# Kernel optimization log

Hardware: AMD Instinct MI355X
Metric: run time of the kernel (lower is better)

## Reference

```python
import jax, jax.numpy as jnp
import numpy as np

B, T_ENC, D_IN, H, C, STEPS = 512, 64, 512, 512, 38, 26


def setup_inputs() -> dict:
    key = jax.random.key(0)
    ks = jax.random.split(key, 12)
    s = 0.05
    return {
        "encoder_output": jax.random.normal(ks[0], (B, T_ENC, D_IN), jnp.float32),
        "text": jax.random.randint(ks[1], (B, STEPS), 0, C),
        "w_i2h": jax.random.normal(ks[2], (H, D_IN), jnp.float32) * s,
        "w_h2h": jax.random.normal(ks[3], (H, H), jnp.float32) * s,
        "b_h2h": jax.random.normal(ks[4], (H,), jnp.float32) * s,
        "w_score": jax.random.normal(ks[5], (1, H), jnp.float32) * s,
        "w_ih": jax.random.normal(ks[6], (4 * H, D_IN + C), jnp.float32) * s,
        "w_hh": jax.random.normal(ks[7], (4 * H, H), jnp.float32) * s,
        "b_ih": jax.random.normal(ks[8], (4 * H,), jnp.float32) * s,
        "b_hh": jax.random.normal(ks[9], (4 * H,), jnp.float32) * s,
        "w_gen": jax.random.normal(ks[10], (C, H), jnp.float32) * s,
        "b_gen": jax.random.normal(ks[11], (C,), jnp.float32) * s,
    }


def reference(encoder_output, text, w_i2h, w_h2h, b_h2h, w_score, w_ih, w_hh,
              b_ih, b_hh, w_gen, b_gen):
    # i2h(batch_H) is step-invariant -> hoist out of the decode loop (same math).
    H_proj = jnp.einsum('btd,hd->bth', encoder_output, w_i2h)  # [B,T,H]
    onehots = jax.nn.one_hot(text, C, dtype=encoder_output.dtype)  # [B,S,C]
    oh_seq = jnp.swapaxes(onehots, 0, 1)  # [S,B,C]

    def step(carry, oh):
        h, c = carry
        hp = (h @ w_h2h.T + b_h2h)[:, None, :]                 # [B,1,H]
        e = jnp.tanh(H_proj + hp) @ w_score[0]                  # [B,T]
        alpha = jax.nn.softmax(e, axis=1)                       # [B,T]
        context = jnp.einsum('bt,btd->bd', alpha, encoder_output)
        x = jnp.concatenate([context, oh], axis=1)              # [B,D+C]
        gates = x @ w_ih.T + b_ih + h @ w_hh.T + b_hh           # [B,4H]
        i_g, f_g, g_g, o_g = jnp.split(gates, 4, axis=1)
        c_new = jax.nn.sigmoid(f_g) * c + jax.nn.sigmoid(i_g) * jnp.tanh(g_g)
        h_new = jax.nn.sigmoid(o_g) * jnp.tanh(c_new)
        return (h_new, c_new), h_new

    z = jnp.zeros((encoder_output.shape[0], w_h2h.shape[0]), encoder_output.dtype)
    _, hs = jax.lax.scan(step, (z, z), oh_seq)                  # hs: [S,B,H]
    hiddens = jnp.swapaxes(hs, 0, 1)                            # [B,S,H]
    probs = hiddens @ w_gen.T + b_gen                           # [B,S,C]
    return probs
```

## Files before the change

### kernel.cpp

```cpp
#include <hip/hip_runtime.h>

typedef __attribute__((ext_vector_type(8))) short bf16x8;
typedef __attribute__((ext_vector_type(4))) float f32x4;
typedef __attribute__((ext_vector_type(4))) int   i32x4;

#define DEV static __device__ __forceinline__

constexpr int BATCH = 512;
constexpr int TENC  = 64;
constexpr int DIN   = 512;
constexpr int HDIM  = 512;
constexpr int NCLS  = 38;
constexpr int STEPS = 26;
constexpr int NG    = 4 * HDIM;

constexpr size_t HP_OFF   = 0;
constexpr size_t HP_SZ    = (size_t)BATCH * TENC * HDIM * 2;
constexpr size_t ENC_OFF  = HP_OFF + HP_SZ;
constexpr size_t ENC_SZ   = (size_t)BATCH * TENC * DIN * 2;
constexpr size_t A2_OFF   = ENC_OFF + ENC_SZ;
constexpr size_t A2_SZ    = (size_t)2 * BATCH * 1024 * 2;
constexpr size_t HP32_OFF = A2_OFF + A2_SZ;
constexpr size_t HP32_SZ  = (size_t)BATCH * HDIM * 4;
constexpr size_t B2R_OFF  = HP32_OFF + HP32_SZ;
constexpr size_t B2R_SZ   = (size_t)NG * 1024 * 2;
constexpr size_t WI2H_OFF = B2R_OFF + B2R_SZ;
constexpr size_t WI2H_SZ  = (size_t)HDIM * DIN * 2;
constexpr size_t B3_OFF   = WI2H_OFF + WI2H_SZ;
constexpr size_t B3_SZ    = (size_t)576 * HDIM * 2;
constexpr size_t WOH_OFF  = B3_OFF + B3_SZ;
constexpr size_t WOH_SZ   = (size_t)NG * NCLS * 4;
constexpr size_t BIAS_OFF = WOH_OFF + WOH_SZ;
constexpr size_t BIAS_SZ  = (size_t)NG * 4;
constexpr size_t HSEQ_OFF = BIAS_OFF + BIAS_SZ;
constexpr size_t HSEQ_SZ  = (size_t)STEPS * BATCH * HDIM * 2;
constexpr size_t BAR_OFF  = HSEQ_OFF + HSEQ_SZ;
constexpr size_t BAR_SZ   = 16384;

DEV float bf2f(unsigned short s) {
    unsigned u = ((unsigned)s) << 16;
    return __builtin_bit_cast(float, u);
}
DEV unsigned short f2bf(float f) {
    unsigned u = __builtin_bit_cast(unsigned, f);
    u = (u + 0x7fffu + ((u >> 16) & 1u)) >> 16;
    return (unsigned short)u;
}
DEV float sigmoid_f(float x) { return 1.f / (1.f + __expf(-x)); }
DEV float tanh_f(float x) {
    x = fminf(fmaxf(x, -15.f), 15.f);
    float e = __expf(2.f * x);
    return (e - 1.f) / (e + 1.f);
}

DEV unsigned aload(const unsigned* p) {
    return __hip_atomic_load(p, __ATOMIC_RELAXED, __HIP_MEMORY_SCOPE_AGENT);
}
DEV unsigned long long aload64(const unsigned long long* p) {
    return __hip_atomic_load(p, __ATOMIC_RELAXED, __HIP_MEMORY_SCOPE_AGENT);
}
DEV float aloadf(const float* p) {
    return __hip_atomic_load(p, __ATOMIC_RELAXED, __HIP_MEMORY_SCOPE_AGENT);
}
DEV void astore(unsigned* p, unsigned v) {
    __hip_atomic_store(p, v, __ATOMIC_RELAXED, __HIP_MEMORY_SCOPE_AGENT);
}
DEV void astoref(float* p, float v) {
    __hip_atomic_store(p, v, __ATOMIC_RELAXED, __HIP_MEMORY_SCOPE_AGENT);
}
DEV bf16x8 mk_frag(unsigned long long lo, unsigned long long hi) {
    union { unsigned long long q[2]; bf16x8 v; } u;
    u.q[0] = lo; u.q[1] = hi;
    return u.v;
}

DEV void gbar(unsigned* bar, int bid) {
    __syncthreads();
    if (threadIdx.x == 0) {
        const int sg = bid & 31;
        unsigned* sub  = bar + sg * 32;
        unsigned* root = bar + 1024;
        unsigned* genp = bar + 1056 + sg * 32;
        unsigned g = aload(genp);
        bool flipped = false;
        if (__hip_atomic_fetch_add(sub, 1u, __ATOMIC_RELAXED, __HIP_MEMORY_SCOPE_AGENT) == 7u) {
            if (__hip_atomic_fetch_add(root, 1u, __ATOMIC_RELAXED, __HIP_MEMORY_SCOPE_AGENT) == 31u) {
                #pragma unroll
                for (int i = 0; i < 32; i++) astore(bar + i * 32, 0u);
                astore(root, 0u);
                asm volatile("s_waitcnt vmcnt(0)" ::: "memory");
                #pragma unroll
                for (int i = 0; i < 32; i++) astore(bar + 1056 + i * 32, g + 1u);
                flipped = true;
            }
        }
        if (!flipped) {
            while (aload(genp) == g) __builtin_amdgcn_s_sleep(1);
        }
    }
    __syncthreads();
}

__global__ void conv_bf16_kernel(const float* __restrict__ in,
                                 unsigned short* __restrict__ out, int n4) {
    int i = blockIdx.x * blockDim.x + threadIdx.x;
    int stride = gridDim.x * blockDim.x;
    for (; i < n4; i += stride) {
        float4 v = ((const float4*)in)[i];
        ushort4 o;
        o.x = f2bf(v.x); o.y = f2bf(v.y); o.z = f2bf(v.z); o.w = f2bf(v.w);
        ((ushort4*)out)[i] = o;
    }
}

__global__ void build_b2r_kernel(const float* __restrict__ w_ih, const float* __restrict__ w_hh,
                                 const float* __restrict__ b_ih, const float* __restrict__ b_hh,
                                 unsigned short* __restrict__ B2r, float* __restrict__ woh,
                                 float* __restrict__ bias2r) {
    int np = blockIdx.x;
    int u = np >> 2, g = np & 3;
    int src = g * 512 + u;
    for (int k = threadIdx.x; k < 512; k += blockDim.x) {
        B2r[np * 1024 + k]       = f2bf(w_ih[src * 550 + k]);
        B2r[np * 1024 + 512 + k] = f2bf(w_hh[src * 512 + k]);
    }
    if (threadIdx.x < NCLS) woh[np * NCLS + threadIdx.x] = w_ih[src * 550 + 512 + threadIdx.x];
    if (threadIdx.x == 0)   bias2r[np] = b_ih[src] + b_hh[src];
}

__global__ void build_b3_kernel(const float* __restrict__ w_h2h, const float* __restrict__ w_gen,
                                unsigned short* __restrict__ B3) {
    int n = blockIdx.x;
    for (int k = threadIdx.x; k < 512; k += blockDim.x) {
        float v = 0.f;
        if (n < 512)      v = w_h2h[n * 512 + k];
        else if (n < 550) v = w_gen[(n - 512) * 512 + k];
        B3[n * 512 + k] = f2bf(v);
    }
}

__global__ void init_state_kernel(float* __restrict__ hp32,
                                  unsigned short* __restrict__ A2,
                                  const float* __restrict__ b_h2h,
                                  unsigned* __restrict__ bar) {
    int b = blockIdx.x;
    for (int j = threadIdx.x; j < 512; j += blockDim.x) {
        hp32[b * 512 + j] = b_h2h[j];
        A2[b * 1024 + 512 + j] = 0;
    }
    if (b == 0)
        for (int j = threadIdx.x; j < 2112; j += blockDim.x) bar[j] = 0;
}

template<int BM, int BN, int WN, int FRM, int FRN>
DEV void gemm_core(const unsigned short* __restrict__ A, int ldA,
                   const unsigned short* __restrict__ Bm, int ldB, int K,
                   int m0, int n0, unsigned short* __restrict__ lA,
                   unsigned short* __restrict__ lB, f32x4 acc[FRM][FRN]) {
    constexpr int LSTR = 40;
    const int tid  = threadIdx.x;
    const int lane = tid & 63;
    const int wid  = tid >> 6;
    const int wm = wid / WN, wn = wid % WN;
    const int fr_row = lane & 15;
    const int fr_kb  = (lane >> 4) * 8;

    for (int k0 = 0; k0 < K; k0 += 32) {
        for (int u = tid; u < BM * 4; u += 256) {
            int r = u >> 2, cb = u & 3;
            *(i32x4*)(lA + r * LSTR + cb * 8) =
                *(const i32x4*)(A + (size_t)(m0 + r) * ldA + k0 + cb * 8);
        }
        for (int u = tid; u < BN * 4; u += 256) {
            int r = u >> 2, cb = u & 3;
            *(i32x4*)(lB + r * LSTR + cb * 8) =
                *(const i32x4*)(Bm + (size_t)(n0 + r) * ldB + k0 + cb * 8);
        }
        __syncthreads();
        bf16x8 af[FRM], bfv[FRN];
        #pragma unroll
        for (int i = 0; i < FRM; i++)
            af[i] = *(const bf16x8*)(lA + (wm * FRM * 16 + i * 16 + fr_row) * LSTR + fr_kb);
        #pragma unroll
        for (int j = 0; j < FRN; j++)
            bfv[j] = *(const bf16x8*)(lB + (wn * FRN * 16 + j * 16 + fr_row) * LSTR + fr_kb);
        #pragma unroll
        for (int i = 0; i < FRM; i++)
            #pragma unroll
            for (int j = 0; j < FRN; j++)
                acc[i][j] = __builtin_amdgcn_mfma_f32_16x16x32_bf16(af[i], bfv[j], acc[i][j], 0, 0, 0);
        __syncthreads();
    }
}

__global__ __launch_bounds__(256) void gemm_bf16out_kernel(
    const unsigned short* __restrict__ A, int ldA,
    const unsigned short* __restrict__ Bm, int ldB,
    unsigned short* __restrict__ C, int ldC, int K) {
    constexpr int BM = 128, BN = 128, FRM = 4, FRN = 4;
    __shared__ __align__(16) unsigned short lA[BM * 40], lB[BN * 40];
    int m0 = blockIdx.x * BM, n0 = blockIdx.y * BN;
    f32x4 acc[FRM][FRN] = {};
    gemm_core<BM, BN, 2, FRM, FRN>(A, ldA, Bm, ldB, K, m0, n0, lA, lB, acc);
    const int lane = threadIdx.x & 63, wid = threadIdx.x >> 6;
    const int wm = wid >> 1, wn = wid & 1;
    #pragma unroll
    for (int i = 0; i < FRM; i++)
        #pragma unroll
        for (int j = 0; j < FRN; j++)
            #pragma unroll
            for (int r = 0; r < 4; r++) {
                int m = m0 + wm * FRM * 16 + i * 16 + (lane >> 4) * 4 + r;
                int n = n0 + wn * FRN * 16 + j * 16 + (lane & 15);
                C[(size_t)m * ldC + n] = f2bf(acc[i][j][r]);
            }
}

__global__ __launch_bounds__(256) void probs_kernel(
    const unsigned short* __restrict__ hseq,
    const unsigned short* __restrict__ Bg,
    const float* __restrict__ b_gen, float* __restrict__ out) {
    __shared__ __align__(16) unsigned short lA[64 * 40], lB[64 * 40];
    int m0 = blockIdx.x * 64;
    f32x4 acc[2][2] = {};
    gemm_core<64, 64, 2, 2, 2>(hseq, 512, Bg, 512, 512, m0, 0, lA, lB, acc);
    const int lane = threadIdx.x & 63, wid = threadIdx.x >> 6;
    const int wm = wid >> 1, wn = wid & 1;
    #pragma unroll
    for (int i = 0; i < 2; i++)
        #pragma unroll
        for (int j = 0; j < 2; j++)
            #pragma unroll
            for (int r = 0; r < 4; r++) {
                int m = m0 + wm * 32 + i * 16 + (lane >> 4) * 4 + r;
                int n = wn * 32 + j * 16 + (lane & 15);
                if (n < NCLS) {
                    int ss = m >> 9, b = m & 511;
                    out[((size_t)b * STEPS + ss) * NCLS + n] = acc[i][j][r] + b_gen[n];
                }
            }
}

__global__ __launch_bounds__(512, 2) void decode_kernel(
    const unsigned short* __restrict__ Hp,
    const unsigned short* __restrict__ enc,
    unsigned short* __restrict__ A2,
    float* __restrict__ hp32,
    const unsigned short* __restrict__ B2r,
    const float* __restrict__ bias2r,
    const float* __restrict__ woh,
    const unsigned short* __restrict__ B3,
    const float* __restrict__ b_h2h,
    const float* __restrict__ w_score,
    const int* __restrict__ text,
    unsigned short* __restrict__ hseq,
    unsigned* __restrict__ bar) {
    __shared__ __align__(16) unsigned short lB2[32 * 1032];
    __shared__ __align__(16) unsigned short lB3[32 * 520];
    __shared__ __align__(16) char scr[18432];

    const int bid  = blockIdx.x;
    const int tid  = threadIdx.x;
    const int lane = tid & 63, wid = tid >> 6;

    const int nb = bid & 63;
    const int mb = bid >> 6;
    const int n3 = bid & 15;
    const int m3 = bid >> 4;

    for (int u = tid; u < 4096; u += 512) {
        int r = u >> 7, cb = u & 127;
        *(i32x4*)(lB2 + r * 1032 + cb * 8) =
            *(const i32x4*)(B2r + (size_t)(nb * 32 + r) * 1024 + cb * 8);
    }
    for (int u = tid; u < 2048; u += 512) {
        int r = u >> 6, cb = u & 63;
        *(i32x4*)(lB3 + r * 520 + cb * 8) =
            *(const i32x4*)(B3 + (size_t)(n3 * 32 + r) * 512 + cb * 8);
    }

    float c0 = 0.f, c1 = 0.f;

    for (int s = 0; s < STEPS; ++s) {
        unsigned short* A2cur = A2 + (size_t)(s & 1) * BATCH * 1024;
        unsigned short* A2nxt = A2 + (size_t)((s + 1) & 1) * BATCH * 1024;

        {
            float* e_lds  = (float*)scr;
            float* al_lds = e_lds + 128;
            const int half = tid >> 8, t4 = tid & 255, w4 = t4 >> 6;
            const int b = bid * 2 + half;
            float hp8[8], ws8[8];
            const float* hpr = hp32 + b * 512 + lane * 8;
            #pragma unroll
            for (int j = 0; j < 8; j++) hp8[j] = aloadf(hpr + j);
            {
                const float4* wsp = (const float4*)(w_score + lane * 8);
                float4 w0 = wsp[0], w1 = wsp[1];
                ws8[0] = w0.x; ws8[1] = w0.y; ws8[2] = w0.z; ws8[3] = w0.w;
                ws8[4] = w1.x; ws8[5] = w1.y; ws8[6] = w1.z; ws8[7] = w1.w;
            }
            for (int t = w4; t < 64; t += 4) {
                bf16x8 hv = *(const bf16x8*)(Hp + ((size_t)b * 64 + t) * 512 + lane * 8);
                float a = 0.f;
                #pragma unroll
                for (int j = 0; j < 8; j++)
                    a += ws8[j] * tanh_f(hp8[j] + bf2f((unsigned short)hv[j]));
                #pragma unroll
                for (int off = 32; off > 0; off >>= 1) a += __shfl_down(a, off);
                if (lane == 0) e_lds[half * 64 + t] = a;
            }
            __syncthreads();
            if (w4 == 0) {
                float v = e_lds[half * 64 + lane];
                float m = v;
                #pragma unroll
                for (int off = 32; off > 0; off >>= 1) m = fmaxf(m, __shfl_xor(m, off));
                float ex = __expf(v - m);
                float sum = ex;
                #pragma unroll
                for (int off = 32; off > 0; off >>= 1) sum += __shfl_xor(sum, off);
                al_lds[half * 64 + lane] = ex / sum;
            }
            __syncthreads();
            float a0 = 0.f, a1 = 0.f;
            const unsigned short* erow = enc + (size_t)b * 64 * 512 + t4 * 2;
            #pragma unroll 8
            for (int t = 0; t < 64; t++) {
                float al = al_lds[half * 64 + t];
                unsigned pv = *(const unsigned*)(erow + (size_t)t * 512);
                a0 += al * bf2f((unsigned short)(pv & 0xffffu));
                a1 += al * bf2f((unsigned short)(pv >> 16));
            }
            unsigned pk = ((unsigned)f2bf(a1) << 16) | (unsigned)f2bf(a0);
            astore((unsigned*)(A2cur + (size_t)b * 1024) + t4, pk);
        }
        gbar(bar, bid);

        {
            const int m0 = mb * 128;
            const unsigned long long* Ab = (const unsigned long long*)
                (A2cur + (size_t)(m0 + wid * 16 + (lane & 15)) * 1024 + (lane >> 4) * 8);
            const unsigned short* lb0 = lB2 + (lane & 15) * 1032 + (lane >> 4) * 8;
            const unsigned short* lb1 = lb0 + 16 * 1032;
            f32x4 acc0 = {}, acc1 = {};
            #pragma unroll
            for (int hf = 0; hf < 2; ++hf) {
                unsigned long long a0v[16], a1v[16];
                #pragma unroll
                for (int kc = 0; kc < 16; ++kc) {
                    a0v[kc] = aload64(Ab + (hf * 16 + kc) * 8);
                    a1v[kc] = aload64(Ab + (hf * 16 + kc) * 8 + 1);
                }
                #pragma unroll
                for (int kc = 0; kc < 16; ++kc) {
                    bf16x8 af = mk_frag(a0v[kc], a1v[kc]);
                    bf16x8 b0 = *(const bf16x8*)(lb0 + (hf * 16 + kc) * 32);
                    bf16x8 b1 = *(const bf16x8*)(lb1 + (hf * 16 + kc) * 32);
                    acc0 = __builtin_amdgcn_mfma_f32_16x16x32_bf16(af, b0, acc0, 0, 0, 0);
                    acc1 = __builtin_amdgcn_mfma_f32_16x16x32_bf16(af, b1, acc1, 0, 0, 0);
                }
            }
            float* gbuf = (float*)scr;
            const int grow = wid * 16 + (lane >> 4) * 4;
            const int gcol = lane & 15;
            #pragma unroll
            for (int r = 0; r < 4; r++) {
                gbuf[(grow + r) * 36 + gcol]      = acc0[r];
                gbuf[(grow + r) * 36 + 16 + gcol] = acc1[r];
            }
            __syncthreads();
            {
                const int rl = tid >> 2, q = tid & 3;
                const int b = m0 + rl;
                const int npb = nb * 32 + q * 8;
                const int u0 = npb >> 2;
                const int tb = text[b * STEPS + s];
                const float* gr = gbuf + rl * 36 + q * 8;
                float4 g0 = *(const float4*)gr;
                float4 g1 = *(const float4*)(gr + 4);
                float vi0 = g0.x + bias2r[npb + 0] + woh[(npb + 0) * NCLS + tb];
                float vf0 = g0.y + bias2r[npb + 1] + woh[(npb + 1) * NCLS + tb];
                float vg0 = g0.z + bias2r[npb + 2] + woh[(npb + 2) * NCLS + tb];
                float vo0 = g0.w + bias2r[npb + 3] + woh[(npb + 3) * NCLS + tb];
                float vi1 = g1.x + bias2r[npb + 4] + woh[(npb + 4) * NCLS + tb];
                float vf1 = g1.y + bias2r[npb + 5] + woh[(npb + 5) * NCLS + tb];
                float vg1 = g1.z + bias2r[npb + 6] + woh[(npb + 6) * NCLS + tb];
                float vo1 = g1.w + bias2r[npb + 7] + woh[(npb + 7) * NCLS + tb];
                float cn0 = sigmoid_f(vf0) * c0 + sigmoid_f(vi0) * tanh_f(vg0);
                float cn1 = sigmoid_f(vf1) * c1 + sigmoid_f(vi1) * tanh_f(vg1);
                c0 = cn0; c1 = cn1;
                float hn0 = sigmoid_f(vo0) * tanh_f(cn0);
                float hn1 = sigmoid_f(vo1) * tanh_f(cn1);
                unsigned hp2 = ((unsigned)f2bf(hn1) << 16) | (unsigned)f2bf(hn0);
                astore((unsigned*)(A2nxt + (size_t)b * 1024 + 512 + u0), hp2);
                *(unsigned*)(hseq + ((size_t)s * BATCH + b) * 512 + u0) = hp2;
            }
        }

        if (s + 1 < STEPS) {
            gbar(bar, bid);
            {
                const int wi = wid & 3, kl = wid >> 2;
                const int tm = (wi >> 1) * 16, tn = (wi & 1) * 16;
                const int m0 = m3 * 32, nc = n3 * 32;
                const unsigned long long* Ab = (const unsigned long long*)
                    (A2nxt + (size_t)(m0 + tm + (lane & 15)) * 1024 + 512 + kl * 256 + (lane >> 4) * 8);
                const unsigned short* lbr = lB3 + (tn + (lane & 15)) * 520 + kl * 256 + (lane >> 4) * 8;
                unsigned long long a0v[8], a1v[8];
                #pragma unroll
                for (int kc = 0; kc < 8; ++kc) {
                    a0v[kc] = aload64(Ab + kc * 8);
                    a1v[kc] = aload64(Ab + kc * 8 + 1);
                }
                f32x4 acc = {};
                #pragma unroll
                for (int kc = 0; kc < 8; ++kc) {
                    bf16x8 af = mk_frag(a0v[kc], a1v[kc]);
                    bf16x8 bf = *(const bf16x8*)(lbr + kc * 32);
                    acc = __builtin_amdgcn_mfma_f32_16x16x32_bf16(af, bf, acc, 0, 0, 0);
                }
                float* pbuf = (float*)scr;
                if (kl == 1) {
                    #pragma unroll
                    for (int r = 0; r < 4; r++)
                        pbuf[wi * 272 + ((lane >> 4) * 4 + r) * 17 + (lane & 15)] = acc[r];
                }
                __syncthreads();
                if (kl == 0) {
                    #pragma unroll
                    for (int r = 0; r < 4; r++) {
                        int row = (lane >> 4) * 4 + r, col = lane & 15;
                        float v = acc[r] + pbuf[wi * 272 + row * 17 + col] + b_h2h[nc + tn + col];
                        astoref(hp32 + (size_t)(m0 + tm + row) * 512 + nc + tn + col, v);
                    }
                }
            }
            gbar(bar, bid);
        }
    }
}

extern "C" void kernel_launch(void* const* d_in, const int* in_sizes, int n_in,
                              void* d_out, int out_size, void* d_ws, size_t ws_size,
                              hipStream_t stream) {
    (void)in_sizes; (void)n_in; (void)out_size; (void)ws_size;
    const float* enc_f   = (const float*)d_in[0];
    const int*   text    = (const int*)d_in[1];
    const float* w_i2h   = (const float*)d_in[2];
    const float* w_h2h   = (const float*)d_in[3];
    const float* b_h2h   = (const float*)d_in[4];
    const float* w_score = (const float*)d_in[5];
    const float* w_ih    = (const float*)d_in[6];
    const float* w_hh    = (const float*)d_in[7];
    const float* b_ih    = (const float*)d_in[8];
    const float* b_hh    = (const float*)d_in[9];
    const float* w_gen   = (const float*)d_in[10];
    const float* b_gen   = (const float*)d_in[11];
    float* out = (float*)d_out;

    char* ws = (char*)d_ws;
    const unsigned short* Hp     = (const unsigned short*)(ws + HP_OFF);
    unsigned short*       Hp_w   = (unsigned short*)(ws + HP_OFF);
    const unsigned short* encb   = (const unsigned short*)(ws + ENC_OFF);
    unsigned short*       encb_w = (unsigned short*)(ws + ENC_OFF);
    unsigned short*       A2     = (unsigned short*)(ws + A2_OFF);
    float*                hp32   = (float*)(ws + HP32_OFF);
    const unsigned short* B2r    = (const unsigned short*)(ws + B2R_OFF);
    unsigned short*       B2r_w  = (unsigned short*)(ws + B2R_OFF);
    unsigned short*       wi2hb  = (unsigned short*)(ws + WI2H_OFF);
    const unsigned short* B3     = (const unsigned short*)(ws + B3_OFF);
    unsigned short*       B3_w   = (unsigned short*)(ws + B3_OFF);
    const float*          woh    = (const float*)(ws + WOH_OFF);
    float*                woh_w  = (float*)(ws + WOH_OFF);
    const float*          bias2r = (const float*)(ws + BIAS_OFF);
    float*                bias2r_w = (float*)(ws + BIAS_OFF);
    unsigned short*       hseq   = (unsigned short*)(ws + HSEQ_OFF);
    unsigned*             bar    = (unsigned*)(ws + BAR_OFF);

    conv_bf16_kernel<<<2048, 256, 0, stream>>>(enc_f, encb_w, BATCH * TENC * DIN / 4);
    conv_bf16_kernel<<<256, 256, 0, stream>>>(w_i2h, wi2hb, HDIM * DIN / 4);
    build_b2r_kernel<<<NG, 256, 0, stream>>>(w_ih, w_hh, b_ih, b_hh, B2r_w, woh_w, bias2r_w);
    build_b3_kernel<<<576, 256, 0, stream>>>(w_h2h, w_gen, B3_w);
    init_state_kernel<<<BATCH, 256, 0, stream>>>(hp32, A2, b_h2h, bar);

    gemm_bf16out_kernel<<<dim3(BATCH * TENC / 128, HDIM / 128), 256, 0, stream>>>(
        encb, DIN, wi2hb, DIN, Hp_w, HDIM, DIN);

    {
        void* args[13] = {
            (void*)&Hp, (void*)&encb, (void*)&A2, (void*)&hp32,
            (void*)&B2r, (void*)&bias2r, (void*)&woh, (void*)&B3,
            (void*)&b_h2h, (void*)&w_score, (void*)&text, (void*)&hseq, (void*)&bar
        };
        hipLaunchCooperativeKernel((const void*)decode_kernel, dim3(256), dim3(512),
                                   args, 0, stream);
    }

    probs_kernel<<<dim3(STEPS * BATCH / 64), 256, 0, stream>>>(
        hseq, B3 + (size_t)512 * 512, b_gen, out);
}
```

Before: 1.358 ms.

## Precompute recurrent gate GEMM half before barrier and use monotonic grid barrier

Moves the h_prev × W_hh half of the gate MFMA accumulation ahead of the attention phase so it overlaps with attention work instead of following the grid barrier. The grid barrier is rewritten to use monotonically increasing generation counters, dropping the per-barrier reset stores and sleep in the spin loop. This relies on the barrier memory being zeroed at each launch and adds register pressure from holding accumulators across the attention phase.

```diff
diff --git a/kernel.cpp b/kernel.cpp
--- a/kernel.cpp
+++ b/kernel.cpp
@@ -74,29 +74,20 @@
     return u.v;
 }
 
-DEV void gbar(unsigned* bar, int bid) {
+DEV void gbar(unsigned* bar, int bid, unsigned g) {
     __syncthreads();
     if (threadIdx.x == 0) {
         const int sg = bid & 31;
         unsigned* sub  = bar + sg * 32;
         unsigned* root = bar + 1024;
         unsigned* genp = bar + 1056 + sg * 32;
-        unsigned g = aload(genp);
-        bool flipped = false;
-        if (__hip_atomic_fetch_add(sub, 1u, __ATOMIC_RELAXED, __HIP_MEMORY_SCOPE_AGENT) == 7u) {
-            if (__hip_atomic_fetch_add(root, 1u, __ATOMIC_RELAXED, __HIP_MEMORY_SCOPE_AGENT) == 31u) {
-                #pragma unroll
-                for (int i = 0; i < 32; i++) astore(bar + i * 32, 0u);
-                astore(root, 0u);
-                asm volatile("s_waitcnt vmcnt(0)" ::: "memory");
-                #pragma unroll
-                for (int i = 0; i < 32; i++) astore(bar + 1056 + i * 32, g + 1u);
-                flipped = true;
-            }
-        }
-        if (!flipped) {
-            while (aload(genp) == g) __builtin_amdgcn_s_sleep(1);
-        }
+        if (__hip_atomic_fetch_add(sub, 1u, __ATOMIC_RELAXED, __HIP_MEMORY_SCOPE_AGENT) == g * 8u - 1u) {
+            if (__hip_atomic_fetch_add(root, 1u, __ATOMIC_RELAXED, __HIP_MEMORY_SCOPE_AGENT) == g * 32u - 1u) {
+                #pragma unroll
+                for (int i = 0; i < 32; i++) astore(bar + 1056 + i * 32, g);
+            }
+        }
+        while (aload(genp) < g) { }
     }
     __syncthreads();
 }
@@ -278,12 +269,39 @@
         *(i32x4*)(lB3 + r * 520 + cb * 8) =
             *(const i32x4*)(B3 + (size_t)(n3 * 32 + r) * 512 + cb * 8);
     }
+    __syncthreads();
 
     float c0 = 0.f, c1 = 0.f;
+    unsigned gen = 0;
+
+    const unsigned short* lb0 = lB2 + (lane & 15) * 1032 + (lane >> 4) * 8;
+    const unsigned short* lb1 = lb0 + 16 * 1032;
+    const int gm0 = mb * 128;
+    const size_t arow_off = (size_t)(gm0 + wid * 16 + (lane & 15)) * 1024 + (lane >> 4) * 8;
 
     for (int s = 0; s < STEPS; ++s) {
         unsigned short* A2cur = A2 + (size_t)(s & 1) * BATCH * 1024;
         unsigned short* A2nxt = A2 + (size_t)((s + 1) & 1) * BATCH * 1024;
+
+        f32x4 acc0 = {}, acc1 = {};
+
+        {
+            const unsigned long long* Ab = (const unsigned long long*)(A2cur + arow_off);
+            unsigned long long a0v[16], a1v[16];
+            #pragma unroll
+            for (int kc = 0; kc < 16; ++kc) {
+                a0v[kc] = aload64(Ab + (16 + kc) * 8);
+                a1v[kc] = aload64(Ab + (16 + kc) * 8 + 1);
+            }
+            #pragma unroll
+            for (int kc = 0; kc < 16; ++kc) {
+                bf16x8 af = mk_frag(a0v[kc], a1v[kc]);
+                bf16x8 b0 = *(const bf16x8*)(lb0 + (16 + kc) * 32);
+                bf16x8 b1 = *(const bf16x8*)(lb1 + (16 + kc) * 32);
+                acc0 = __builtin_amdgcn_mfma_f32_16x16x32_bf16(af, b0, acc0, 0, 0, 0);
+                acc1 = __builtin_amdgcn_mfma_f32_16x16x32_bf16(af, b1, acc1, 0, 0, 0);
+            }
+        }
 
         {
             float* e_lds  = (float*)scr;
@@ -335,31 +353,23 @@
             unsigned pk = ((unsigned)f2bf(a1) << 16) | (unsigned)f2bf(a0);
             astore((unsigned*)(A2cur + (size_t)b * 1024) + t4, pk);
         }
-        gbar(bar, bid);
+        gbar(bar, bid, ++gen);
 
         {
-            const int m0 = mb * 128;
-            const unsigned long long* Ab = (const unsigned long long*)
-                (A2cur + (size_t)(m0 + wid * 16 + (lane & 15)) * 1024 + (lane >> 4) * 8);
-            const unsigned short* lb0 = lB2 + (lane & 15) * 1032 + (lane >> 4) * 8;
-            const unsigned short* lb1 = lb0 + 16 * 1032;
-            f32x4 acc0 = {}, acc1 = {};
-            #pragma unroll
-            for (int hf = 0; hf < 2; ++hf) {
-                unsigned long long a0v[16], a1v[16];
-                #pragma unroll
-                for (int kc = 0; kc < 16; ++kc) {
-                    a0v[kc] = aload64(Ab + (hf * 16 + kc) * 8);
-                    a1v[kc] = aload64(Ab + (hf * 16 + kc) * 8 + 1);
-                }
-                #pragma unroll
-                for (int kc = 0; kc < 16; ++kc) {
-                    bf16x8 af = mk_frag(a0v[kc], a1v[kc]);
-                    bf16x8 b0 = *(const bf16x8*)(lb0 + (hf * 16 + kc) * 32);
-                    bf16x8 b1 = *(const bf16x8*)(lb1 + (hf * 16 + kc) * 32);
-                    acc0 = __builtin_amdgcn_mfma_f32_16x16x32_bf16(af, b0, acc0, 0, 0, 0);
-                    acc1 = __builtin_amdgcn_mfma_f32_16x16x32_bf16(af, b1, acc1, 0, 0, 0);
-                }
+            const unsigned long long* Ab = (const unsigned long long*)(A2cur + arow_off);
+            unsigned long long a0v[16], a1v[16];
+            #pragma unroll
+            for (int kc = 0; kc < 16; ++kc) {
+                a0v[kc] = aload64(Ab + kc * 8);
+                a1v[kc] = aload64(Ab + kc * 8 + 1);
+            }
+            #pragma unroll
+            for (int kc = 0; kc < 16; ++kc) {
+                bf16x8 af = mk_frag(a0v[kc], a1v[kc]);
+                bf16x8 b0 = *(const bf16x8*)(lb0 + kc * 32);
+                bf16x8 b1 = *(const bf16x8*)(lb1 + kc * 32);
+                acc0 = __builtin_amdgcn_mfma_f32_16x16x32_bf16(af, b0, acc0, 0, 0, 0);
+                acc1 = __builtin_amdgcn_mfma_f32_16x16x32_bf16(af, b1, acc1, 0, 0, 0);
             }
             float* gbuf = (float*)scr;
             const int grow = wid * 16 + (lane >> 4) * 4;
@@ -372,7 +382,7 @@
             __syncthreads();
             {
                 const int rl = tid >> 2, q = tid & 3;
-                const int b = m0 + rl;
+                const int b = gm0 + rl;
                 const int npb = nb * 32 + q * 8;
                 const int u0 = npb >> 2;
                 const int tb = text[b * STEPS + s];
@@ -399,7 +409,7 @@
         }
 
         if (s + 1 < STEPS) {
-            gbar(bar, bid);
+            gbar(bar, bid, ++gen);
             {
                 const int wi = wid & 3, kl = wid >> 2;
                 const int tm = (wi >> 1) * 16, tn = (wi & 1) * 16;
@@ -436,7 +446,7 @@
                     }
                 }
             }
-            gbar(bar, bid);
+            gbar(bar, bid, ++gen);
         }
     }
 }
```

Measured after the change: 1.595 ms (median of 2 runs). +17.4%, slower.
